# Performance work log

Measured on AMD Instinct MI355X. Metric: run time of the kernel, lower is better.

The kernel has to match this reference:

```python
import jax, jax.numpy as jnp
import numpy as np

B, T, C, H = 8, 2048, 256, 4
D = C // H  # head_dim = 64
SCALE = D ** -0.5


def setup_inputs() -> dict:
    key = jax.random.key(0)
    ks = jax.random.split(key, 5)
    return {
        "x": jax.random.normal(ks[0], (B, T, C), dtype=jnp.float32),
        "Wqkv": jax.random.normal(ks[1], (C, 3 * C), dtype=jnp.float32) * (C ** -0.5),
        "bqkv": jax.random.normal(ks[2], (3 * C,), dtype=jnp.float32) * 0.02,
        "Wproj": jax.random.normal(ks[3], (C, C), dtype=jnp.float32) * (C ** -0.5),
        "bproj": jax.random.normal(ks[4], (C,), dtype=jnp.float32) * 0.02,
    }


def reference(x, Wqkv, bqkv, Wproj, bproj):
    b, t, c = x.shape
    # QKV projection -> (3, B, H, T, D) matching torch permute(2,0,3,1,4)
    qkv = (x @ Wqkv + bqkv).reshape(b, t, 3, H, D)
    qkv = jnp.transpose(qkv, (2, 0, 3, 1, 4))
    q, k, v = qkv[0], qkv[1], qkv[2]  # each (B, H, T, D)
    # Full T x T scores (faithful to the original non-fused implementation)
    attn = jnp.einsum("bhqd,bhkd->bhqk", q, k) * SCALE
    causal = jnp.triu(jnp.ones((t, t), dtype=bool), k=1)  # True above diagonal
    attn = jnp.where(causal, -jnp.inf, attn)
    attn = jax.nn.softmax(attn, axis=-1)
    # dropout is identity in eval mode
    out = jnp.einsum("bhqk,bhkd->bhqd", attn, v)  # (B, H, T, D)
    out = jnp.transpose(out, (0, 2, 1, 3)).reshape(b, t, c)
    return out @ Wproj + bproj
```

## Files before the change

### kernel.cpp

```cpp
#include <hip/hip_runtime.h>
#include <hip/hip_bf16.h>
#include <math.h>

#define BATCH 8
#define SEQ   2048
#define CH    256
#define NH    4
#define HD    64
#define NQB   (SEQ / 64)
#define QSCALE 0.18033688011112042f

typedef short  bfrag __attribute__((ext_vector_type(8)));
typedef float  ffrag __attribute__((ext_vector_type(4)));
typedef unsigned short ushort_t;

__device__ __forceinline__ unsigned short f2bf(float f) {
    union { float f; unsigned int u; } v; v.f = f;
    unsigned int r = v.u + 0x7FFF + ((v.u >> 16) & 1);
    return (unsigned short)(r >> 16);
}

#define XN  (BATCH * SEQ * CH / 4)
#define WQN (CH * 3 * CH)
#define WPN (CH * CH)

__global__ __launch_bounds__(256) void prep_kernel(
    const float* __restrict__ x, const float* __restrict__ Wqkv,
    const float* __restrict__ Wproj,
    ushort_t* __restrict__ xb, ushort_t* __restrict__ WqkvT,
    ushort_t* __restrict__ WprojT) {
    const int fid = blockIdx.x * 256 + threadIdx.x;
    if (fid < XN) {
        const float4 v = ((const float4*)x)[fid];
        ushort4 p;
        p.x = f2bf(v.x); p.y = f2bf(v.y); p.z = f2bf(v.z); p.w = f2bf(v.w);
        ((ushort4*)xb)[fid] = p;
    } else if (fid < XN + WQN) {
        const int i = fid - XN;
        const int n = i >> 8, k = i & 255;
        WqkvT[n * CH + k] = f2bf(Wqkv[k * (3 * CH) + n]);
    } else if (fid < XN + WQN + WPN) {
        const int i = fid - XN - WQN;
        const int n = i >> 8, k = i & 255;
        WprojT[n * CH + k] = f2bf(Wproj[k * CH + n]);
    }
}

#define GLS 72

__global__ __launch_bounds__(256) void qkv_mfma_kernel(
    const ushort_t* __restrict__ xb, const ushort_t* __restrict__ Wt,
    const float* __restrict__ bias,
    ushort_t* __restrict__ Qb, ushort_t* __restrict__ Kb,
    ushort_t* __restrict__ Vtb) {
    __shared__ ushort_t smem[2 * 128 * GLS];
    ushort_t* As = smem;
    ushort_t* Bs = smem + 128 * GLS;

    const int tid = threadIdx.x;
    const int wv  = tid >> 6;
    const int ln  = tid & 63;
    const int l15 = ln & 15;
    const int l4  = ln >> 4;
    const int wr  = wv >> 1;
    const int wc  = wv & 1;
    const int n0  = blockIdx.x * 128;
    const int m0  = blockIdx.y * 128;

    ffrag acc[4][4];
    #pragma unroll
    for (int i = 0; i < 4; i++)
        #pragma unroll
        for (int j = 0; j < 4; j++) acc[i][j] = (ffrag){0.f, 0.f, 0.f, 0.f};

    for (int k0 = 0; k0 < CH; k0 += 64) {
        #pragma unroll
        for (int r = 0; r < 4; r++) {
            const int fid = tid + r * 256;
            const int row = fid >> 3, c8 = (fid & 7) * 8;
            *(uint4*)&As[row * GLS + c8] = *(const uint4*)&xb[(m0 + row) * CH + k0 + c8];
            *(uint4*)&Bs[row * GLS + c8] = *(const uint4*)&Wt[(n0 + row) * CH + k0 + c8];
        }
        __syncthreads();
        #pragma unroll
        for (int kk = 0; kk < 64; kk += 32) {
            bfrag a[4], b[4];
            #pragma unroll
            for (int i = 0; i < 4; i++)
                a[i] = *(const bfrag*)&As[(wr * 64 + i * 16 + l15) * GLS + kk + l4 * 8];
            #pragma unroll
            for (int j = 0; j < 4; j++)
                b[j] = *(const bfrag*)&Bs[(wc * 64 + j * 16 + l15) * GLS + kk + l4 * 8];
            #pragma unroll
            for (int i = 0; i < 4; i++)
                #pragma unroll
                for (int j = 0; j < 4; j++)
                    acc[i][j] = __builtin_amdgcn_mfma_f32_16x16x32_bf16(a[i], b[j], acc[i][j], 0, 0, 0);
        }
        __syncthreads();
    }

    const int mat = n0 >> 8;
    const int b   = m0 >> 11;
    const int t0  = m0 & (SEQ - 1);
    ushort_t (*T)[136] = (ushort_t(*)[136])smem;

    if (mat < 2) {
        const float sc = (mat == 0) ? QSCALE : 1.0f;
        #pragma unroll
        for (int j = 0; j < 4; j++) {
            const int n_local = wc * 64 + j * 16 + l15;
            const float bj = bias[n0 + n_local];
            #pragma unroll
            for (int i = 0; i < 4; i++) {
                const int m_base = wr * 64 + i * 16 + l4 * 4;
                #pragma unroll
                for (int r = 0; r < 4; r++)
                    T[m_base + r][n_local] = f2bf((acc[i][j][r] + bj) * sc);
            }
        }
        __syncthreads();
        ushort_t* dst = (mat == 0) ? Qb : Kb;
        #pragma unroll
        for (int rr = 0; rr < 8; rr++) {
            const int fid = tid + rr * 256;
            const int row = fid >> 4;
            const int c8  = (fid & 15) * 8;
            const int n_glob = n0 + c8;
            const int h = (n_glob >> 6) & 3;
            const int d = n_glob & 63;
            *(uint4*)&dst[((size_t)((b * NH + h) * SEQ) + t0 + row) * HD + d] =
                *(const uint4*)&T[row][c8];
        }
    } else {
        #pragma unroll
        for (int j = 0; j < 4; j++) {
            const int n_local = wc * 64 + j * 16 + l15;
            const float bj = bias[n0 + n_local];
            #pragma unroll
            for (int i = 0; i < 4; i++) {
                const int m_base = wr * 64 + i * 16 + l4 * 4;
                ushort4 pk;
                pk.x = f2bf(acc[i][j][0] + bj);
                pk.y = f2bf(acc[i][j][1] + bj);
                pk.z = f2bf(acc[i][j][2] + bj);
                pk.w = f2bf(acc[i][j][3] + bj);
                *(ushort4*)&T[n_local][m_base] = pk;
            }
        }
        __syncthreads();
        #pragma unroll
        for (int rr = 0; rr < 8; rr++) {
            const int fid = tid + rr * 256;
            const int row = fid >> 4;
            const int c8  = (fid & 15) * 8;
            const int n_glob = n0 + row;
            const int h = (n_glob >> 6) & 3;
            const int d = n_glob & 63;
            *(uint4*)&Vtb[(size_t)((b * NH + h) * HD + d) * SEQ + t0 + c8] =
                *(const uint4*)&T[row][c8];
        }
    }
}

#define LSA 72

__global__ __launch_bounds__(256, 5) void attn_mfma_kernel(
    const ushort_t* __restrict__ Qb, const ushort_t* __restrict__ Kb,
    const ushort_t* __restrict__ Vtb, ushort_t* __restrict__ out) {
    __shared__ ushort_t Qs[64][LSA];
    __shared__ ushort_t Ks[64][LSA];
    __shared__ ushort_t Vts[64][LSA];
    __shared__ float aw[4][16];
    __shared__ float lw[4][16];

    const int tid = threadIdx.x;
    const int wv  = tid >> 6;
    const int ln  = tid & 63;
    const int l15 = ln & 15;
    const int l4  = ln >> 4;

    const int L  = blockIdx.x;
    const int g  = L & 255;
    const int s4 = L >> 8;
    const int v  = g >> 5;
    const int qb = (s4 == 0) ? (31 - v) : (s4 == 1) ? (16 + v) : (s4 == 2) ? (15 - v) : v;
    const int bh = g & 31;
    const int b  = bh >> 2;
    const int h  = bh & 3;

    {
        const ushort_t* Qp = Qb + (size_t)(bh * SEQ + qb * 64) * HD;
        #pragma unroll
        for (int r = 0; r < 2; r++) {
            const int fid = tid + r * 256;
            const int row = fid >> 3, c8 = (fid & 7) * 8;
            *(uint4*)&Qs[row][c8] = *(const uint4*)&Qp[row * HD + c8];
        }
    }

    const ushort_t* Kbase = Kb  + (size_t)bh * SEQ * HD;
    const ushort_t* Vbase = Vtb + (size_t)bh * HD * SEQ;
    const int srow = (tid + 0) >> 3,  sc8a = ((tid + 0) & 7) * 8;
    const int srow2 = (tid + 256) >> 3, sc8b = ((tid + 256) & 7) * 8;
    uint4 kK0, kK1, kV0, kV1;
    kK0 = *(const uint4*)&Kbase[srow  * HD + sc8a];
    kK1 = *(const uint4*)&Kbase[srow2 * HD + sc8b];
    kV0 = *(const uint4*)&Vbase[srow  * SEQ + sc8a];
    kV1 = *(const uint4*)&Vbase[srow2 * SEQ + sc8b];

    __syncthreads();
    const bfrag bq0 = *(const bfrag*)&Qs[wv * 16 + l15][l4 * 8];
    const bfrag bq1 = *(const bfrag*)&Qs[wv * 16 + l15][32 + l4 * 8];

    ffrag o[4];
    #pragma unroll
    for (int n = 0; n < 4; n++) o[n] = (ffrag){0.f, 0.f, 0.f, 0.f};
    float m_q = -INFINITY;
    float l_q = 0.f;

    const int qg_l = qb * 64 + wv * 16 + l15;

    for (int kt = 0; kt <= qb; kt++) {
        *(uint4*)&Ks[srow][sc8a]   = kK0;
        *(uint4*)&Ks[srow2][sc8b]  = kK1;
        *(uint4*)&Vts[srow][sc8a]  = kV0;
        *(uint4*)&Vts[srow2][sc8b] = kV1;
        __syncthreads();

        if (kt < qb) {
            const ushort_t* Kp  = Kbase + (size_t)(kt + 1) * 64 * HD;
            const ushort_t* Vtp = Vbase + (kt + 1) * 64;
            kK0 = *(const uint4*)&Kp[srow  * HD + sc8a];
            kK1 = *(const uint4*)&Kp[srow2 * HD + sc8b];
            kV0 = *(const uint4*)&Vtp[srow  * SEQ + sc8a];
            kV1 = *(const uint4*)&Vtp[srow2 * SEQ + sc8b];
        }

        ffrag s[4];
        #pragma unroll
        for (int n = 0; n < 4; n++) {
            const bfrag ak0 = *(const bfrag*)&Ks[n * 16 + l15][l4 * 8];
            const bfrag ak1 = *(const bfrag*)&Ks[n * 16 + l15][32 + l4 * 8];
            ffrag z = (ffrag){0.f, 0.f, 0.f, 0.f};
            z = __builtin_amdgcn_mfma_f32_16x16x32_bf16(ak0, bq0, z, 0, 0, 0);
            z = __builtin_amdgcn_mfma_f32_16x16x32_bf16(ak1, bq1, z, 0, 0, 0);
            s[n] = z;
        }
        if (kt == qb) {
            #pragma unroll
            for (int n = 0; n < 4; n++)
                #pragma unroll
                for (int r = 0; r < 4; r++)
                    if (kt * 64 + n * 16 + l4 * 4 + r > qg_l) s[n][r] = -INFINITY;
        }

        float mx = s[0][0];
        #pragma unroll
        for (int n = 0; n < 4; n++)
            #pragma unroll
            for (int r = 0; r < 4; r++) mx = fmaxf(mx, s[n][r]);
        mx = fmaxf(mx, __shfl_xor(mx, 16));
        mx = fmaxf(mx, __shfl_xor(mx, 32));
        const float mo = m_q;
        const float mn = fmaxf(mo, mx);
        const float alpha = __builtin_amdgcn_exp2f(mo - mn);
        m_q = mn;

        float rs = 0.f;
        #pragma unroll
        for (int n = 0; n < 4; n++)
            #pragma unroll
            for (int r = 0; r < 4; r++) {
                const float p = __builtin_amdgcn_exp2f(s[n][r] - mn);
                s[n][r] = p;
                rs += p;
            }
        rs += __shfl_xor(rs, 16);
        rs += __shfl_xor(rs, 32);
        l_q = l_q * alpha + rs;

        if (l4 == 0) aw[wv][l15] = alpha;

        #pragma unroll
        for (int n = 0; n < 4; n++) {
            const __hip_bfloat162 pa = __float22bfloat162_rn(make_float2(s[n][0], s[n][1]));
            const __hip_bfloat162 pb = __float22bfloat162_rn(make_float2(s[n][2], s[n][3]));
            uint2 pk;
            pk.x = *(const unsigned int*)&pa;
            pk.y = *(const unsigned int*)&pb;
            *(uint2*)&Qs[wv * 16 + l15][n * 16 + l4 * 4] = pk;
        }

        const float4 al4 = *(const float4*)&aw[wv][l4 * 4];
        const float alr[4] = {al4.x, al4.y, al4.z, al4.w};
        #pragma unroll
        for (int n = 0; n < 4; n++)
            #pragma unroll
            for (int r = 0; r < 4; r++) o[n][r] *= alr[r];

        const bfrag ap0 = *(const bfrag*)&Qs[wv * 16 + l15][l4 * 8];
        const bfrag ap1 = *(const bfrag*)&Qs[wv * 16 + l15][32 + l4 * 8];
        #pragma unroll
        for (int n = 0; n < 4; n++) {
            const bfrag bv0 = *(const bfrag*)&Vts[n * 16 + l15][l4 * 8];
            const bfrag bv1 = *(const bfrag*)&Vts[n * 16 + l15][32 + l4 * 8];
            o[n] = __builtin_amdgcn_mfma_f32_16x16x32_bf16(ap0, bv0, o[n], 0, 0, 0);
            o[n] = __builtin_amdgcn_mfma_f32_16x16x32_bf16(ap1, bv1, o[n], 0, 0, 0);
        }
        __syncthreads();
    }

    if (l4 == 0) lw[wv][l15] = l_q;
    const float4 lv4 = *(const float4*)&lw[wv][l4 * 4];
    const float lvr[4] = {1.f / lv4.x, 1.f / lv4.y, 1.f / lv4.z, 1.f / lv4.w};
    const int tg = qb * 64 + wv * 16 + l4 * 4;
    ushort_t* op = out + (size_t)(b * SEQ) * CH + h * HD;
    #pragma unroll
    for (int n = 0; n < 4; n++)
        #pragma unroll
        for (int r = 0; r < 4; r++)
            op[(size_t)(tg + r) * CH + n * 16 + l15] = f2bf(o[n][r] * lvr[r]);
}

__global__ __launch_bounds__(256) void proj_mfma_kernel(
    const ushort_t* __restrict__ Ab, const ushort_t* __restrict__ Wt,
    const float* __restrict__ bias, float* __restrict__ O) {
    __shared__ ushort_t smem[2 * 128 * GLS];
    ushort_t* As = smem;
    ushort_t* Bs = smem + 128 * GLS;

    const int tid = threadIdx.x;
    const int wv  = tid >> 6;
    const int ln  = tid & 63;
    const int l15 = ln & 15;
    const int l4  = ln >> 4;
    const int wr  = wv >> 1;
    const int wc  = wv & 1;
    const int n0  = blockIdx.x * 128;
    const int m0  = blockIdx.y * 128;

    ffrag acc[4][4];
    #pragma unroll
    for (int i = 0; i < 4; i++)
        #pragma unroll
        for (int j = 0; j < 4; j++) acc[i][j] = (ffrag){0.f, 0.f, 0.f, 0.f};

    for (int k0 = 0; k0 < CH; k0 += 64) {
        #pragma unroll
        for (int r = 0; r < 4; r++) {
            const int fid = tid + r * 256;
            const int row = fid >> 3, c8 = (fid & 7) * 8;
            *(uint4*)&As[row * GLS + c8] = *(const uint4*)&Ab[(m0 + row) * CH + k0 + c8];
            *(uint4*)&Bs[row * GLS + c8] = *(const uint4*)&Wt[(n0 + row) * CH + k0 + c8];
        }
        __syncthreads();
        #pragma unroll
        for (int kk = 0; kk < 64; kk += 32) {
            bfrag a[4], b[4];
            #pragma unroll
            for (int i = 0; i < 4; i++)
                a[i] = *(const bfrag*)&As[(wr * 64 + i * 16 + l15) * GLS + kk + l4 * 8];
            #pragma unroll
            for (int j = 0; j < 4; j++)
                b[j] = *(const bfrag*)&Bs[(wc * 64 + j * 16 + l15) * GLS + kk + l4 * 8];
            #pragma unroll
            for (int i = 0; i < 4; i++)
                #pragma unroll
                for (int j = 0; j < 4; j++)
                    acc[i][j] = __builtin_amdgcn_mfma_f32_16x16x32_bf16(a[i], b[j], acc[i][j], 0, 0, 0);
        }
        __syncthreads();
    }

    #pragma unroll
    for (int j = 0; j < 4; j++) {
        const int n = n0 + wc * 64 + j * 16 + l15;
        const float bj = bias[n];
        #pragma unroll
        for (int i = 0; i < 4; i++) {
            const int m = m0 + wr * 64 + i * 16 + l4 * 4;
            #pragma unroll
            for (int r = 0; r < 4; r++)
                O[(size_t)(m + r) * CH + n] = acc[i][j][r] + bj;
        }
    }
}

extern "C" void kernel_launch(void* const* d_in, const int* in_sizes, int n_in,
                              void* d_out, int out_size, void* d_ws, size_t ws_size,
                              hipStream_t stream) {
    const float* x     = (const float*)d_in[0];
    const float* Wqkv  = (const float*)d_in[1];
    const float* bqkv  = (const float*)d_in[2];
    const float* Wproj = (const float*)d_in[3];
    const float* bproj = (const float*)d_in[4];
    float* out = (float*)d_out;

    const size_t BHTD = (size_t)BATCH * NH * SEQ * HD;
    ushort_t* xb     = (ushort_t*)d_ws;
    ushort_t* WqkvT  = xb + BHTD;
    ushort_t* WprojT = WqkvT + (size_t)3 * CH * CH;
    ushort_t* Qb     = WprojT + (size_t)CH * CH;
    ushort_t* Kb     = Qb + BHTD;
    ushort_t* Vtb    = Kb + BHTD;
    ushort_t* attn_b = Vtb + BHTD;

    const int M = BATCH * SEQ;

    {
        const int total = XN + WQN + WPN;
        prep_kernel<<<(total + 255) / 256, 256, 0, stream>>>(x, Wqkv, Wproj, xb, WqkvT, WprojT);
    }
    {
        dim3 grid((3 * CH) / 128, M / 128);
        qkv_mfma_kernel<<<grid, 256, 0, stream>>>(xb, WqkvT, bqkv, Qb, Kb, Vtb);
    }
    {
        attn_mfma_kernel<<<dim3(NQB * BATCH * NH), 256, 0, stream>>>(Qb, Kb, Vtb, attn_b);
    }
    {
        dim3 grid(CH / 128, M / 128);
        proj_mfma_kernel<<<grid, 256, 0, stream>>>(attn_b, WprojT, bproj, out);
    }
}
```

Measured before the change: 145.4 us.

## Fuse x bf16 conversion into QKV GEMM, restructure attention smem, narrow proj tiles

The separate pass that converts x to bf16 is removed; the QKV GEMM now loads fp32 x and packs it to bf16 while staging into shared memory, which saves a full read and write of x. The attention kernel double-buffers K/V in XOR-swizzled shared memory with a single barrier per tile, loads Q fragments straight from global memory, and broadcasts alpha and l with shuffles instead of shared arrays. Its occupancy hint drops from 5 to 4 blocks. The projection GEMM uses 64-wide N tiles to launch more blocks, at the cost of less data reuse per block.

New measurement: 144.2 us. No clear change (-0.9%).

```diff
diff --git a/kernel.cpp b/kernel.cpp
--- a/kernel.cpp
+++ b/kernel.cpp
@@ -19,28 +19,23 @@
     unsigned int r = v.u + 0x7FFF + ((v.u >> 16) & 1);
     return (unsigned short)(r >> 16);
 }
-
-#define XN  (BATCH * SEQ * CH / 4)
+__device__ __forceinline__ unsigned int pack2(float a, float b) {
+    const __hip_bfloat162 p = __float22bfloat162_rn(make_float2(a, b));
+    return *(const unsigned int*)&p;
+}
+
 #define WQN (CH * 3 * CH)
 #define WPN (CH * CH)
 
 __global__ __launch_bounds__(256) void prep_kernel(
-    const float* __restrict__ x, const float* __restrict__ Wqkv,
-    const float* __restrict__ Wproj,
-    ushort_t* __restrict__ xb, ushort_t* __restrict__ WqkvT,
-    ushort_t* __restrict__ WprojT) {
+    const float* __restrict__ Wqkv, const float* __restrict__ Wproj,
+    ushort_t* __restrict__ WqkvT, ushort_t* __restrict__ WprojT) {
     const int fid = blockIdx.x * 256 + threadIdx.x;
-    if (fid < XN) {
-        const float4 v = ((const float4*)x)[fid];
-        ushort4 p;
-        p.x = f2bf(v.x); p.y = f2bf(v.y); p.z = f2bf(v.z); p.w = f2bf(v.w);
-        ((ushort4*)xb)[fid] = p;
-    } else if (fid < XN + WQN) {
-        const int i = fid - XN;
-        const int n = i >> 8, k = i & 255;
+    if (fid < WQN) {
+        const int n = fid >> 8, k = fid & 255;
         WqkvT[n * CH + k] = f2bf(Wqkv[k * (3 * CH) + n]);
-    } else if (fid < XN + WQN + WPN) {
-        const int i = fid - XN - WQN;
+    } else if (fid < WQN + WPN) {
+        const int i = fid - WQN;
         const int n = i >> 8, k = i & 255;
         WprojT[n * CH + k] = f2bf(Wproj[k * CH + n]);
     }
@@ -49,7 +44,7 @@
 #define GLS 72
 
 __global__ __launch_bounds__(256) void qkv_mfma_kernel(
-    const ushort_t* __restrict__ xb, const ushort_t* __restrict__ Wt,
+    const float* __restrict__ x, const ushort_t* __restrict__ Wt,
     const float* __restrict__ bias,
     ushort_t* __restrict__ Qb, ushort_t* __restrict__ Kb,
     ushort_t* __restrict__ Vtb) {
@@ -78,7 +73,13 @@
         for (int r = 0; r < 4; r++) {
             const int fid = tid + r * 256;
             const int row = fid >> 3, c8 = (fid & 7) * 8;
-            *(uint4*)&As[row * GLS + c8] = *(const uint4*)&xb[(m0 + row) * CH + k0 + c8];
+            const float* xp = &x[(size_t)(m0 + row) * CH + k0 + c8];
+            const float4 va = *(const float4*)xp;
+            const float4 vb = *(const float4*)(xp + 4);
+            uint4 pk;
+            pk.x = pack2(va.x, va.y); pk.y = pack2(va.z, va.w);
+            pk.z = pack2(vb.x, vb.y); pk.w = pack2(vb.z, vb.w);
+            *(uint4*)&As[row * GLS + c8] = pk;
             *(uint4*)&Bs[row * GLS + c8] = *(const uint4*)&Wt[(n0 + row) * CH + k0 + c8];
         }
         __syncthreads();
@@ -163,22 +164,18 @@
     }
 }
 
-#define LSA 72
-
-__global__ __launch_bounds__(256, 5) void attn_mfma_kernel(
+__global__ __launch_bounds__(256, 4) void attn_mfma_kernel(
     const ushort_t* __restrict__ Qb, const ushort_t* __restrict__ Kb,
     const ushort_t* __restrict__ Vtb, ushort_t* __restrict__ out) {
-    __shared__ ushort_t Qs[64][LSA];
-    __shared__ ushort_t Ks[64][LSA];
-    __shared__ ushort_t Vts[64][LSA];
-    __shared__ float aw[4][16];
-    __shared__ float lw[4][16];
+    __shared__ ushort_t Ps[64 * 64];
+    __shared__ ushort_t KV[4 * 64 * 64];
 
     const int tid = threadIdx.x;
     const int wv  = tid >> 6;
     const int ln  = tid & 63;
     const int l15 = ln & 15;
     const int l4  = ln >> 4;
+    const int e   = l15 & 7;
 
     const int L  = blockIdx.x;
     const int g  = L & 255;
@@ -189,59 +186,72 @@
     const int b  = bh >> 2;
     const int h  = bh & 3;
 
-    {
-        const ushort_t* Qp = Qb + (size_t)(bh * SEQ + qb * 64) * HD;
-        #pragma unroll
-        for (int r = 0; r < 2; r++) {
-            const int fid = tid + r * 256;
-            const int row = fid >> 3, c8 = (fid & 7) * 8;
-            *(uint4*)&Qs[row][c8] = *(const uint4*)&Qp[row * HD + c8];
-        }
-    }
+    const ushort_t* Qp = Qb + ((size_t)(bh * SEQ + qb * 64 + wv * 16 + l15)) * HD + l4 * 8;
+    const bfrag bq0 = *(const bfrag*)Qp;
+    const bfrag bq1 = *(const bfrag*)(Qp + 32);
 
     const ushort_t* Kbase = Kb  + (size_t)bh * SEQ * HD;
     const ushort_t* Vbase = Vtb + (size_t)bh * HD * SEQ;
-    const int srow = (tid + 0) >> 3,  sc8a = ((tid + 0) & 7) * 8;
-    const int srow2 = (tid + 256) >> 3, sc8b = ((tid + 256) & 7) * 8;
+    const int srow  = tid >> 3;
+    const int sc    = tid & 7;
+    const int goffA = srow * 64 + sc * 8;
+    const int voffA = srow * SEQ + sc * 8;
+    const int soffA = srow * 64 + ((sc ^ (srow & 7)) * 8);
+
+    const int kf0 = l15 * 64 + ((l4 ^ e) * 8);
+    const int pf0 = (wv * 16 + l15) * 64 + ((l4 ^ e) * 8);
+    const int pp = e >> 1;
+    const int pwb = (wv * 16 + l15) * 64 + (((l4 >> 1) ^ (e & 1)) * 8) + (l4 & 1) * 4;
+
     uint4 kK0, kK1, kV0, kV1;
-    kK0 = *(const uint4*)&Kbase[srow  * HD + sc8a];
-    kK1 = *(const uint4*)&Kbase[srow2 * HD + sc8b];
-    kV0 = *(const uint4*)&Vbase[srow  * SEQ + sc8a];
-    kV1 = *(const uint4*)&Vbase[srow2 * SEQ + sc8b];
-
-    __syncthreads();
-    const bfrag bq0 = *(const bfrag*)&Qs[wv * 16 + l15][l4 * 8];
-    const bfrag bq1 = *(const bfrag*)&Qs[wv * 16 + l15][32 + l4 * 8];
+    kK0 = *(const uint4*)&Kbase[goffA];
+    kK1 = *(const uint4*)&Kbase[goffA + 32 * 64];
+    kV0 = *(const uint4*)&Vbase[voffA];
+    kV1 = *(const uint4*)&Vbase[voffA + 32 * SEQ];
+    *(uint4*)&KV[soffA]          = kK0;
+    *(uint4*)&KV[soffA + 2048]   = kK1;
+    *(uint4*)&KV[8192 + soffA]        = kV0;
+    *(uint4*)&KV[8192 + soffA + 2048] = kV1;
+    if (qb >= 1) {
+        kK0 = *(const uint4*)&Kbase[4096 + goffA];
+        kK1 = *(const uint4*)&Kbase[4096 + goffA + 32 * 64];
+        kV0 = *(const uint4*)&Vbase[64 + voffA];
+        kV1 = *(const uint4*)&Vbase[64 + voffA + 32 * SEQ];
+    }
 
     ffrag o[4];
     #pragma unroll
     for (int n = 0; n < 4; n++) o[n] = (ffrag){0.f, 0.f, 0.f, 0.f};
     float m_q = -INFINITY;
     float l_q = 0.f;
-
     const int qg_l = qb * 64 + wv * 16 + l15;
 
     for (int kt = 0; kt <= qb; kt++) {
-        *(uint4*)&Ks[srow][sc8a]   = kK0;
-        *(uint4*)&Ks[srow2][sc8b]  = kK1;
-        *(uint4*)&Vts[srow][sc8a]  = kV0;
-        *(uint4*)&Vts[srow2][sc8b] = kV1;
-        __syncthreads();
-
-        if (kt < qb) {
-            const ushort_t* Kp  = Kbase + (size_t)(kt + 1) * 64 * HD;
-            const ushort_t* Vtp = Vbase + (kt + 1) * 64;
-            kK0 = *(const uint4*)&Kp[srow  * HD + sc8a];
-            kK1 = *(const uint4*)&Kp[srow2 * HD + sc8b];
-            kV0 = *(const uint4*)&Vtp[srow  * SEQ + sc8a];
-            kV1 = *(const uint4*)&Vtp[srow2 * SEQ + sc8b];
-        }
+        if (kt > 0) {
+            const int kb = (kt & 1) * 4096;
+            *(uint4*)&KV[kb + soffA]          = kK0;
+            *(uint4*)&KV[kb + soffA + 2048]   = kK1;
+            *(uint4*)&KV[8192 + kb + soffA]        = kV0;
+            *(uint4*)&KV[8192 + kb + soffA + 2048] = kV1;
+            if (kt < qb) {
+                const ushort_t* Kp  = Kbase + (kt + 1) * 4096;
+                const ushort_t* Vtp = Vbase + (kt + 1) * 64;
+                kK0 = *(const uint4*)&Kp[goffA];
+                kK1 = *(const uint4*)&Kp[goffA + 32 * 64];
+                kV0 = *(const uint4*)&Vtp[voffA];
+                kV1 = *(const uint4*)&Vtp[voffA + 32 * SEQ];
+            }
+        }
+        __syncthreads();
+
+        const ushort_t* Kbuf = KV + (kt & 1) * 4096;
+        const ushort_t* Vbuf = KV + 8192 + (kt & 1) * 4096;
 
         ffrag s[4];
         #pragma unroll
         for (int n = 0; n < 4; n++) {
-            const bfrag ak0 = *(const bfrag*)&Ks[n * 16 + l15][l4 * 8];
-            const bfrag ak1 = *(const bfrag*)&Ks[n * 16 + l15][32 + l4 * 8];
+            const bfrag ak0 = *(const bfrag*)&Kbuf[n * 1024 + kf0];
+            const bfrag ak1 = *(const bfrag*)&Kbuf[n * 1024 + (kf0 ^ 32)];
             ffrag z = (ffrag){0.f, 0.f, 0.f, 0.f};
             z = __builtin_amdgcn_mfma_f32_16x16x32_bf16(ak0, bq0, z, 0, 0, 0);
             z = __builtin_amdgcn_mfma_f32_16x16x32_bf16(ak1, bq1, z, 0, 0, 0);
@@ -262,9 +272,8 @@
             for (int r = 0; r < 4; r++) mx = fmaxf(mx, s[n][r]);
         mx = fmaxf(mx, __shfl_xor(mx, 16));
         mx = fmaxf(mx, __shfl_xor(mx, 32));
-        const float mo = m_q;
-        const float mn = fmaxf(mo, mx);
-        const float alpha = __builtin_amdgcn_exp2f(mo - mn);
+        const float mn = fmaxf(m_q, mx);
+        const float alpha = __builtin_amdgcn_exp2f(m_q - mn);
         m_q = mn;
 
         float rs = 0.f;
@@ -280,53 +289,48 @@
         rs += __shfl_xor(rs, 32);
         l_q = l_q * alpha + rs;
 
-        if (l4 == 0) aw[wv][l15] = alpha;
-
         #pragma unroll
         for (int n = 0; n < 4; n++) {
-            const __hip_bfloat162 pa = __float22bfloat162_rn(make_float2(s[n][0], s[n][1]));
-            const __hip_bfloat162 pb = __float22bfloat162_rn(make_float2(s[n][2], s[n][3]));
             uint2 pk;
-            pk.x = *(const unsigned int*)&pa;
-            pk.y = *(const unsigned int*)&pb;
-            *(uint2*)&Qs[wv * 16 + l15][n * 16 + l4 * 4] = pk;
-        }
-
-        const float4 al4 = *(const float4*)&aw[wv][l4 * 4];
-        const float alr[4] = {al4.x, al4.y, al4.z, al4.w};
-        #pragma unroll
-        for (int n = 0; n < 4; n++)
-            #pragma unroll
-            for (int r = 0; r < 4; r++) o[n][r] *= alr[r];
-
-        const bfrag ap0 = *(const bfrag*)&Qs[wv * 16 + l15][l4 * 8];
-        const bfrag ap1 = *(const bfrag*)&Qs[wv * 16 + l15][32 + l4 * 8];
+            pk.x = pack2(s[n][0], s[n][1]);
+            pk.y = pack2(s[n][2], s[n][3]);
+            *(uint2*)&Ps[pwb + ((n ^ pp) << 4)] = pk;
+        }
+
+        #pragma unroll
+        for (int r = 0; r < 4; r++) {
+            const float ar = __shfl(alpha, l4 * 20 + r);
+            #pragma unroll
+            for (int n = 0; n < 4; n++) o[n][r] *= ar;
+        }
+
+        const bfrag ap0 = *(const bfrag*)&Ps[pf0];
+        const bfrag ap1 = *(const bfrag*)&Ps[pf0 ^ 32];
         #pragma unroll
         for (int n = 0; n < 4; n++) {
-            const bfrag bv0 = *(const bfrag*)&Vts[n * 16 + l15][l4 * 8];
-            const bfrag bv1 = *(const bfrag*)&Vts[n * 16 + l15][32 + l4 * 8];
+            const bfrag bv0 = *(const bfrag*)&Vbuf[n * 1024 + kf0];
+            const bfrag bv1 = *(const bfrag*)&Vbuf[n * 1024 + (kf0 ^ 32)];
             o[n] = __builtin_amdgcn_mfma_f32_16x16x32_bf16(ap0, bv0, o[n], 0, 0, 0);
             o[n] = __builtin_amdgcn_mfma_f32_16x16x32_bf16(ap1, bv1, o[n], 0, 0, 0);
         }
-        __syncthreads();
-    }
-
-    if (l4 == 0) lw[wv][l15] = l_q;
-    const float4 lv4 = *(const float4*)&lw[wv][l4 * 4];
-    const float lvr[4] = {1.f / lv4.x, 1.f / lv4.y, 1.f / lv4.z, 1.f / lv4.w};
+    }
+
     const int tg = qb * 64 + wv * 16 + l4 * 4;
     ushort_t* op = out + (size_t)(b * SEQ) * CH + h * HD;
     #pragma unroll
-    for (int n = 0; n < 4; n++)
-        #pragma unroll
-        for (int r = 0; r < 4; r++)
-            op[(size_t)(tg + r) * CH + n * 16 + l15] = f2bf(o[n][r] * lvr[r]);
+    for (int r = 0; r < 4; r++) {
+        const float lr = __shfl(l_q, l4 * 20 + r);
+        const float li = 1.0f / lr;
+        #pragma unroll
+        for (int n = 0; n < 4; n++)
+            op[(size_t)(tg + r) * CH + n * 16 + l15] = f2bf(o[n][r] * li);
+    }
 }
 
 __global__ __launch_bounds__(256) void proj_mfma_kernel(
     const ushort_t* __restrict__ Ab, const ushort_t* __restrict__ Wt,
     const float* __restrict__ bias, float* __restrict__ O) {
-    __shared__ ushort_t smem[2 * 128 * GLS];
+    __shared__ ushort_t smem[(128 + 64) * GLS];
     ushort_t* As = smem;
     ushort_t* Bs = smem + 128 * GLS;
 
@@ -337,45 +341,50 @@
     const int l4  = ln >> 4;
     const int wr  = wv >> 1;
     const int wc  = wv & 1;
-    const int n0  = blockIdx.x * 128;
+    const int n0  = blockIdx.x * 64;
     const int m0  = blockIdx.y * 128;
 
-    ffrag acc[4][4];
+    ffrag acc[4][2];
     #pragma unroll
     for (int i = 0; i < 4; i++)
         #pragma unroll
-        for (int j = 0; j < 4; j++) acc[i][j] = (ffrag){0.f, 0.f, 0.f, 0.f};
+        for (int j = 0; j < 2; j++) acc[i][j] = (ffrag){0.f, 0.f, 0.f, 0.f};
 
     for (int k0 = 0; k0 < CH; k0 += 64) {
         #pragma unroll
         for (int r = 0; r < 4; r++) {
             const int fid = tid + r * 256;
             const int row = fid >> 3, c8 = (fid & 7) * 8;
-            *(uint4*)&As[row * GLS + c8] = *(const uint4*)&Ab[(m0 + row) * CH + k0 + c8];
+            *(uint4*)&As[row * GLS + c8] = *(const uint4*)&Ab[(size_t)(m0 + row) * CH + k0 + c8];
+        }
+        #pragma unroll
+        for (int r = 0; r < 2; r++) {
+            const int fid = tid + r * 256;
+            const int row = fid >> 3, c8 = (fid & 7) * 8;
             *(uint4*)&Bs[row * GLS + c8] = *(const uint4*)&Wt[(n0 + row) * CH + k0 + c8];
         }
         __syncthreads();
         #pragma unroll
         for (int kk = 0; kk < 64; kk += 32) {
-            bfrag a[4], b[4];
+            bfrag a[4], b[2];
             #pragma unroll
             for (int i = 0; i < 4; i++)
                 a[i] = *(const bfrag*)&As[(wr * 64 + i * 16 + l15) * GLS + kk + l4 * 8];
             #pragma unroll
-            for (int j = 0; j < 4; j++)
-                b[j] = *(const bfrag*)&Bs[(wc * 64 + j * 16 + l15) * GLS + kk + l4 * 8];
+            for (int j = 0; j < 2; j++)
+                b[j] = *(const bfrag*)&Bs[(wc * 32 + j * 16 + l15) * GLS + kk + l4 * 8];
             #pragma unroll
             for (int i = 0; i < 4; i++)
                 #pragma unroll
-                for (int j = 0; j < 4; j++)
+                for (int j = 0; j < 2; j++)
                     acc[i][j] = __builtin_amdgcn_mfma_f32_16x16x32_bf16(a[i], b[j], acc[i][j], 0, 0, 0);
         }
         __syncthreads();
     }
 
     #pragma unroll
-    for (int j = 0; j < 4; j++) {
-        const int n = n0 + wc * 64 + j * 16 + l15;
+    for (int j = 0; j < 2; j++) {
+        const int n = n0 + wc * 32 + j * 16 + l15;
         const float bj = bias[n];
         #pragma unroll
         for (int i = 0; i < 4; i++) {
@@ -398,8 +407,7 @@
     float* out = (float*)d_out;
 
     const size_t BHTD = (size_t)BATCH * NH * SEQ * HD;
-    ushort_t* xb     = (ushort_t*)d_ws;
-    ushort_t* WqkvT  = xb + BHTD;
+    ushort_t* WqkvT  = (ushort_t*)d_ws;
     ushort_t* WprojT = WqkvT + (size_t)3 * CH * CH;
     ushort_t* Qb     = WprojT + (size_t)CH * CH;
     ushort_t* Kb     = Qb + BHTD;
@@ -409,18 +417,18 @@
     const int M = BATCH * SEQ;
 
     {
-        const int total = XN + WQN + WPN;
-        prep_kernel<<<(total + 255) / 256, 256, 0, stream>>>(x, Wqkv, Wproj, xb, WqkvT, WprojT);
+        const int total = WQN + WPN;
+        prep_kernel<<<(total + 255) / 256, 256, 0, stream>>>(Wqkv, Wproj, WqkvT, WprojT);
     }
     {
         dim3 grid((3 * CH) / 128, M / 128);
-        qkv_mfma_kernel<<<grid, 256, 0, stream>>>(xb, WqkvT, bqkv, Qb, Kb, Vtb);
+        qkv_mfma_kernel<<<grid, 256, 0, stream>>>(x, WqkvT, bqkv, Qb, Kb, Vtb);
     }
     {
         attn_mfma_kernel<<<dim3(NQB * BATCH * NH), 256, 0, stream>>>(Qb, Kb, Vtb, attn_b);
     }
     {
-        dim3 grid(CH / 128, M / 128);
+        dim3 grid(CH / 64, M / 128);
         proj_mfma_kernel<<<grid, 256, 0, stream>>>(attn_b, WprojT, bproj, out);
     }
 }
```
